# Kernel optimization log

Measured on AMD Instinct MI355X. Metric: run time of the kernel, lower is better.

The kernel has to match this reference:

```python
import jax, jax.numpy as jnp
import numpy as np

V, E, H2 = 32000, 512, 1024  # vocab, embed dim, lstm hidden (hidden_dim*2)
H = 512                      # attention inner dim (hidden_dim)
B, S = 64, 128
L = 2


def _lstm_cell(x, h, c, w_ih, w_hh, b_ih, b_hh):
    # PyTorch gate order: i, f, g, o
    gates = x @ w_ih.T + b_ih + h @ w_hh.T + b_hh
    i, f, g, o = jnp.split(gates, 4, axis=-1)
    i = jax.nn.sigmoid(i); f = jax.nn.sigmoid(f)
    g = jnp.tanh(g); o = jax.nn.sigmoid(o)
    c_new = f * c + i * g
    h_new = o * jnp.tanh(c_new)
    return h_new, c_new


def setup_inputs() -> dict:
    key = jax.random.key(0)
    ks = jax.random.split(key, 20)
    s = 0.05
    inp = {
        'input_token': jax.random.randint(ks[0], (B,), 0, V, dtype=jnp.int32),
        'hidden': jax.random.normal(ks[1], (L, B, H2), jnp.float32),
        'cell': jax.random.normal(ks[2], (L, B, H2), jnp.float32),
        'encoder_outputs': jax.random.normal(ks[3], (B, S, H2), jnp.float32),
        'mask': jax.random.randint(ks[4], (B, S), 0, 2, dtype=jnp.int32),
        'emb_table': jax.random.normal(ks[5], (V, E), jnp.float32) * s,
        'attn_w': jax.random.normal(ks[6], (H, 4 * H), jnp.float32) * s,
        'attn_b': jnp.zeros((H,), jnp.float32),
        'v_w': jax.random.normal(ks[7], (1, H), jnp.float32) * s,
        'w_ih0': jax.random.normal(ks[8], (4 * H2, E + H2), jnp.float32) * s,
        'w_hh0': jax.random.normal(ks[9], (4 * H2, H2), jnp.float32) * s,
        'b_ih0': jnp.zeros((4 * H2,), jnp.float32),
        'b_hh0': jnp.zeros((4 * H2,), jnp.float32),
        'w_ih1': jax.random.normal(ks[10], (4 * H2, H2), jnp.float32) * s,
        'w_hh1': jax.random.normal(ks[11], (4 * H2, H2), jnp.float32) * s,
        'b_ih1': jnp.zeros((4 * H2,), jnp.float32),
        'b_hh1': jnp.zeros((4 * H2,), jnp.float32),
        'fc_w': jax.random.normal(ks[12], (V, 4 * H + E), jnp.float32) * s,
        'fc_b': jnp.zeros((V,), jnp.float32),
    }
    return inp


def reference(input_token, hidden, cell, encoder_outputs, mask,
              emb_table, attn_w, attn_b, v_w,
              w_ih0, w_hh0, b_ih0, b_hh0,
              w_ih1, w_hh1, b_ih1, b_hh1,
              fc_w, fc_b):
    embedded = emb_table[input_token]                       # [B, E]
    h_top = hidden[-1]                                      # [B, 2H]
    # Bahdanau additive attention
    h_rep = jnp.broadcast_to(h_top[:, None, :], (B, S, H2))
    energy = jnp.tanh(jnp.concatenate([h_rep, encoder_outputs], axis=2) @ attn_w.T + attn_b)  # [B,S,H]
    attention = energy @ v_w[0]                             # [B, S]
    attention = jnp.where(mask == 0, jnp.float32(-1e10), attention)
    attn_weights = jax.nn.softmax(attention, axis=1)
    context = jnp.einsum('bs,bsd->bd', attn_weights, encoder_outputs)  # [B, 2H]
    # single-step 2-layer LSTM
    x = jnp.concatenate([embedded, context], axis=1)        # [B, E+2H]
    h0, c0 = _lstm_cell(x, hidden[0], cell[0], w_ih0, w_hh0, b_ih0, b_hh0)
    h1, c1 = _lstm_cell(h0, hidden[1], cell[1], w_ih1, w_hh1, b_ih1, b_hh1)
    new_hidden = jnp.stack([h0, h1])
    new_cell = jnp.stack([c0, c1])
    prediction = jnp.concatenate([h1, context, embedded], axis=1) @ fc_w.T + fc_b  # [B, V]
    return prediction, new_hidden, new_cell, attn_weights
```

## Files before the change

kernel.cpp:

```cpp
#include <hip/hip_runtime.h>


typedef __attribute__((ext_vector_type(8))) short bf16x8;
typedef __attribute__((ext_vector_type(4))) float f32x4;

__device__ __forceinline__ short f2bf(float f){
  __bf16 h = (__bf16)f;
  return __builtin_bit_cast(short, h);
}

__device__ __forceinline__ bf16x8 cvt8(float4 a, float4 b){
  bf16x8 r;
  r[0]=f2bf(a.x); r[1]=f2bf(a.y); r[2]=f2bf(a.z); r[3]=f2bf(a.w);
  r[4]=f2bf(b.x); r[5]=f2bf(b.y); r[6]=f2bf(b.z); r[7]=f2bf(b.w);
  return r;
}

__device__ __forceinline__ bf16x8 ld8_bf(const float* __restrict__ p){
  return cvt8(*(const float4*)p, *(const float4*)(p + 4));
}

__device__ __forceinline__ float fast_tanh(float x){
  x = fminf(fmaxf(x, -15.f), 15.f);
  float t = __expf(2.f * x);
  return (t - 1.f) / (t + 1.f);
}
__device__ __forceinline__ float fast_sig(float x){
  return 1.f / (1.f + __expf(-x));
}

__device__ __forceinline__ void stage16(const void* src, void* dst_lds){
  __builtin_amdgcn_global_load_lds(
      (const __attribute__((address_space(1))) void*)src,
      (__attribute__((address_space(3))) void*)dst_lds, 16, 0, 0);
}

__global__ __launch_bounds__(256) void prep_all(
    const int* __restrict__ tok, const float* __restrict__ emb,
    const float* __restrict__ hidden, const float* __restrict__ enc,
    const float* __restrict__ attn_w,
    short* __restrict__ encbf, short* __restrict__ Wbf,
    short* __restrict__ A0, short* __restrict__ A1, short* __restrict__ Zb,
    float* __restrict__ sco)
{
  const int bid = blockIdx.x, t = threadIdx.x;
  if (bid < 4096){
    long i = ((long)bid*256 + t)*8;
    *(bf16x8*)(encbf + i) = ld8_bf(enc + i);
  } else if (bid < 4352){
    int j = (bid-4096)*256 + t;
    int r = j >> 7, c = (j & 127)*8;
    *(bf16x8*)(Wbf + r*1024 + c) = ld8_bf(attn_w + (long)r*2048 + 1024 + c);
  } else if (bid < 4368){
    int j = (bid-4352)*256 + t;
    int b = j >> 6, e8 = (j & 63)*8;
    bf16x8 v = ld8_bf(emb + (long)tok[b]*512 + e8);
    *(bf16x8*)(A0 + b*2560 + e8) = v;
    *(bf16x8*)(Zb + b*2560 + 2048 + e8) = v;
  } else if (bid < 4400){
    int j = (bid-4368)*256 + t;
    int b = j >> 7, n8 = (j & 127)*8;
    *(bf16x8*)(A0 + b*2560 + 1536 + n8) = ld8_bf(hidden + (long)b*1024 + n8);
    *(bf16x8*)(A1 + b*2048 + 1024 + n8) = ld8_bf(hidden + 65536 + (long)b*1024 + n8);
  } else {
    int j = (bid-4400)*256 + t;
    float4 z = {0.f, 0.f, 0.f, 0.f};
    *(float4*)(sco + j*8) = z;
    *(float4*)(sco + j*8 + 4) = z;
  }
}

#define KSL 256
__global__ __launch_bounds__(256) void gemm_lds(
    const short* __restrict__ A, int lda,
    const float* __restrict__ W1, int sW1, int K1,
    const float* __restrict__ W2, int sW2,
    float* __restrict__ P, int N)
{
  __shared__ short Al[64*256];
  __shared__ float Wl[3][64*64];
  const int wv   = threadIdx.x >> 6;
  const int lane = threadIdx.x & 63;
  const int l15  = lane & 15;
  const int lg   = lane >> 4;
  const int nb   = blockIdx.x * 64;
  const int k0   = blockIdx.y * KSL;

  const float* W; int sW, koff;
  if (k0 < K1){ W = W1; sW = sW1; koff = k0; }
  else        { W = W2; sW = sW2; koff = k0 - K1; }

  {
    const int r2  = lane >> 5;
    const int c16 = (lane & 31) * 16;
    #pragma unroll
    for (int i = 0; i < 8; ++i){
      int rbase = wv*16 + i*2;
      int row   = rbase + r2;
      const char* src = (const char*)A + (long)row*lda*2 + (long)k0*2
                        + (c16 ^ ((row & 7) << 4));
      stage16(src, (void*)(Al + rbase*256));
    }
  }

  auto STAGEW = [&](int bi, int kbase){
    #pragma unroll
    for (int i = 0; i < 4; ++i){
      int row = wv*16 + i*4 + lg;
      const char* src = (const char*)(W + (long)(nb + row)*sW + koff + kbase)
                        + ((l15*16) ^ ((row & 7) << 4));
      stage16(src, (void*)&Wl[bi][(wv*16 + i*4)*64]);
    }
  };

  STAGEW(0, 0);
  STAGEW(1, 64);
  asm volatile("s_waitcnt vmcnt(8)" ::: "memory");
  asm volatile("s_barrier" ::: "memory");

  f32x4 acc[4];
  #pragma unroll
  for (int m = 0; m < 4; ++m) acc[m] = (f32x4){0.f,0.f,0.f,0.f};

  const int  rl = wv*16 + l15;
  const int  sw = (l15 & 7) << 4;
  const char* wbase = (const char*)&Wl[0][0];
  const char* abase = (const char*)Al;

  auto COMPUTE = [&](int bi, int t){
    bf16x8 a[4][2];
    #pragma unroll
    for (int m = 0; m < 4; ++m)
      #pragma unroll
      for (int h = 0; h < 2; ++h){
        int cb = t*128 + h*64 + lg*16;
        a[m][h] = *(const bf16x8*)(abase + (m*16 + l15)*512 + (cb ^ sw));
      }
    const char* rb = wbase + bi*16384 + rl*256;
    float4 w00 = *(const float4*)(rb + ((lg*32      ) ^ sw));
    float4 w01 = *(const float4*)(rb + ((lg*32 + 16 ) ^ sw));
    float4 w10 = *(const float4*)(rb + ((lg*32 + 128) ^ sw));
    float4 w11 = *(const float4*)(rb + ((lg*32 + 144) ^ sw));
    bf16x8 wf0 = cvt8(w00, w01);
    bf16x8 wf1 = cvt8(w10, w11);
    #pragma unroll
    for (int m = 0; m < 4; ++m)
      acc[m] = __builtin_amdgcn_mfma_f32_16x16x32_bf16(a[m][0], wf0, acc[m], 0,0,0);
    #pragma unroll
    for (int m = 0; m < 4; ++m)
      acc[m] = __builtin_amdgcn_mfma_f32_16x16x32_bf16(a[m][1], wf1, acc[m], 0,0,0);
  };

  asm volatile("s_waitcnt vmcnt(4)" ::: "memory");
  COMPUTE(0, 0);
  STAGEW(2, 128);
  asm volatile("s_waitcnt vmcnt(4)" ::: "memory");
  COMPUTE(1, 1);
  STAGEW(0, 192);
  asm volatile("s_waitcnt vmcnt(4)" ::: "memory");
  COMPUTE(2, 2);
  asm volatile("s_waitcnt vmcnt(0)" ::: "memory");
  COMPUTE(0, 3);

  float* p = P + (long)blockIdx.y * 64 * N;
  #pragma unroll
  for (int mt = 0; mt < 4; ++mt)
    #pragma unroll
    for (int r = 0; r < 4; ++r){
      int m = mt*16 + lg*4 + r;
      p[(long)m * N + nb + wv*16 + l15] = acc[mt][r];
    }
}

__global__ __launch_bounds__(256) void gemm_fc2(
    const short* __restrict__ A, int lda,
    const float* __restrict__ W, int sW,
    const float* __restrict__ bias,
    float* __restrict__ C, int N)
{
  __shared__ short Al[2][64*128];
  __shared__ float Wl[3][64*64];
  const int wv   = threadIdx.x >> 6;
  const int lane = threadIdx.x & 63;
  const int l15  = lane & 15;
  const int lg   = lane >> 4;
  const int nb   = blockIdx.x * 64;

  auto STAGEA = [&](int c){
    short* dst = Al[c & 1];
    #pragma unroll
    for (int i = 0; i < 4; ++i){
      int rbase = wv*16 + i*4;
      int row   = rbase + lg;
      const char* src = (const char*)(A + (long)row*lda + c*128)
                        + ((l15*16) ^ ((row & 7) << 4));
      stage16(src, (void*)(dst + rbase*128));
    }
  };
  auto STAGEW = [&](int s){
    float* dst = Wl[s % 3];
    #pragma unroll
    for (int i = 0; i < 4; ++i){
      int row = wv*16 + i*4 + lg;
      const char* src = (const char*)(W + (long)(nb + row)*sW + s*64)
                        + ((l15*16) ^ ((row & 7) << 4));
      stage16(src, (void*)(dst + (wv*16 + i*4)*64));
    }
  };

  f32x4 acc[4];
  #pragma unroll
  for (int m = 0; m < 4; ++m) acc[m] = (f32x4){0.f,0.f,0.f,0.f};

  const int rl = wv*16 + l15;
  const int sw = (l15 & 7) << 4;

  auto COMPUTE = [&](int s){
    const char* abase = (const char*)Al[(s >> 1) & 1];
    const int   kh    = (s & 1) * 128;
    bf16x8 a[4][2];
    #pragma unroll
    for (int m = 0; m < 4; ++m)
      #pragma unroll
      for (int h = 0; h < 2; ++h){
        int cb = kh + h*64 + lg*16;
        a[m][h] = *(const bf16x8*)(abase + (m*16 + l15)*256 + (cb ^ sw));
      }
    const char* rb = (const char*)Wl[s % 3] + rl*256;
    float4 w00 = *(const float4*)(rb + ((lg*32      ) ^ sw));
    float4 w01 = *(const float4*)(rb + ((lg*32 + 16 ) ^ sw));
    float4 w10 = *(const float4*)(rb + ((lg*32 + 128) ^ sw));
    float4 w11 = *(const float4*)(rb + ((lg*32 + 144) ^ sw));
    bf16x8 wf0 = cvt8(w00, w01);
    bf16x8 wf1 = cvt8(w10, w11);
    #pragma unroll
    for (int m = 0; m < 4; ++m)
      acc[m] = __builtin_amdgcn_mfma_f32_16x16x32_bf16(a[m][0], wf0, acc[m], 0,0,0);
    #pragma unroll
    for (int m = 0; m < 4; ++m)
      acc[m] = __builtin_amdgcn_mfma_f32_16x16x32_bf16(a[m][1], wf1, acc[m], 0,0,0);
  };

  STAGEA(0); STAGEW(0); STAGEW(1);
  asm volatile("s_waitcnt vmcnt(4)" ::: "memory");
  __builtin_amdgcn_s_barrier();

  STAGEA(1);
  COMPUTE(0);
  STAGEW(2);
  asm volatile("s_waitcnt vmcnt(4)" ::: "memory");
  COMPUTE(1);
  STAGEW(3);
  __builtin_amdgcn_s_barrier();

  for (int c = 1; c < 19; ++c){
    STAGEA(c+1);
    asm volatile("s_waitcnt vmcnt(8)" ::: "memory");
    COMPUTE(2*c);
    STAGEW(2*c+2);
    asm volatile("s_waitcnt vmcnt(4)" ::: "memory");
    COMPUTE(2*c+1);
    STAGEW(2*c+3);
    __builtin_amdgcn_s_barrier();
  }

  asm volatile("s_waitcnt vmcnt(4)" ::: "memory");
  COMPUTE(38);
  asm volatile("s_waitcnt vmcnt(0)" ::: "memory");
  COMPUTE(39);

  const int col = nb + wv*16 + l15;
  const float bn = bias[col];
  #pragma unroll
  for (int mt = 0; mt < 4; ++mt)
    #pragma unroll
    for (int r = 0; r < 4; ++r){
      int m = mt*16 + lg*4 + r;
      C[(long)m * N + col] = acc[mt][r] + bn;
    }
}

__global__ __launch_bounds__(256) void energy_lds(
    const short* __restrict__ encbf, const short* __restrict__ Wbf,
    const float* __restrict__ Ph, const float* __restrict__ attn_b,
    const float* __restrict__ v_w, float* __restrict__ scores)
{
  __shared__ short Ab[3][64*64];
  __shared__ short Bb[3][64*64];
  const int bx   = blockIdx.x;
  const int m3   = bx & 127, n3 = bx >> 7;
  const int wv   = threadIdx.x >> 6;
  const int lane = threadIdx.x & 63;
  const int l15  = lane & 15;
  const int lg   = lane >> 4;
  const int mb   = m3 * 64;
  const int nbg  = n3 * 64;
  const int nb   = nbg + wv * 16;
  const int b    = mb >> 7;

  const int hi = b*512 + nb + l15;
  const float hp = attn_b[nb + l15] + Ph[hi] + Ph[32768 + hi]
                 + Ph[65536 + hi] + Ph[98304 + hi];
  const float vn = v_w[nb + l15];

  const int srow = lane >> 3;
  const int scb  = (lane & 7) * 16;

  auto STAGE = [&](int c, int kb){
    short* da = Ab[c % 3];
    short* db = Bb[c % 3];
    #pragma unroll
    for (int i = 0; i < 2; ++i){
      int rbase = wv*16 + i*8;
      int row   = rbase + srow;
      int swz   = scb ^ ((row & 7) << 4);
      const char* sa = (const char*)(encbf + (long)(mb + row)*1024 + kb) + swz;
      stage16(sa, (void*)(da + rbase*64));
      const char* sb = (const char*)(Wbf + (long)(nbg + row)*1024 + kb) + swz;
      stage16(sb, (void*)(db + rbase*64));
    }
  };

  f32x4 acc[4] = {};
  const int brow = wv*16 + l15;
  const int bswz = (brow & 7) << 4;
  const int aswz = (l15 & 7) << 4;

  auto COMPUTE = [&](int c){
    const char* ab = (const char*)Ab[c % 3];
    const char* bb = (const char*)Bb[c % 3];
    #pragma unroll
    for (int h = 0; h < 2; ++h){
      const int colb = h*64 + lg*16;
      bf16x8 bf_ = *(const bf16x8*)(bb + brow*128 + (colb ^ bswz));
      #pragma unroll
      for (int m = 0; m < 4; ++m){
        const int arow = m*16 + l15;
        bf16x8 af = *(const bf16x8*)(ab + arow*128 + (colb ^ aswz));
        acc[m] = __builtin_amdgcn_mfma_f32_16x16x32_bf16(af, bf_, acc[m], 0,0,0);
      }
    }
  };

  STAGE(0, 0);
  STAGE(1, 64);
  for (int c = 0; c < 14; ++c){
    asm volatile("s_waitcnt vmcnt(4)" ::: "memory");
    __builtin_amdgcn_s_barrier();
    COMPUTE(c);
    STAGE(c+2, (c+2)*64);
  }
  asm volatile("s_waitcnt vmcnt(4)" ::: "memory");
  __builtin_amdgcn_s_barrier();
  COMPUTE(14);
  asm volatile("s_waitcnt vmcnt(0)" ::: "memory");
  __builtin_amdgcn_s_barrier();
  COMPUTE(15);

  #pragma unroll
  for (int mt = 0; mt < 4; ++mt){
    #pragma unroll
    for (int r = 0; r < 4; ++r){
      int m = mb + mt*16 + lg*4 + r;
      float e = fast_tanh(acc[mt][r] + hp) * vn;
      e += __shfl_xor(e, 1, 16);
      e += __shfl_xor(e, 2, 16);
      e += __shfl_xor(e, 4, 16);
      e += __shfl_xor(e, 8, 16);
      if (l15 == 0) atomicAdd(&scores[m], e);
    }
  }
}

__global__ __launch_bounds__(256) void ctxsm_k(
    const float* __restrict__ sco, const int* __restrict__ mask,
    const short* __restrict__ encbf, float* __restrict__ aw,
    short* __restrict__ A0, short* __restrict__ Zb)
{
  const int bb = blockIdx.x;
  const int t  = threadIdx.x;
  __shared__ float red[128];
  __shared__ float w[128];
  float v = 0.f;
  if (t < 128){
    v = sco[bb*128 + t];
    if (mask[bb*128 + t] == 0) v = -1e10f;
    red[t] = v;
  }
  __syncthreads();
  for (int d = 64; d > 0; d >>= 1){
    if (t < d) red[t] = fmaxf(red[t], red[t + d]);
    __syncthreads();
  }
  const float mx = red[0];
  __syncthreads();
  if (t < 128){
    float e = __expf(v - mx);
    w[t] = e; red[t] = e;
  }
  __syncthreads();
  for (int d = 64; d > 0; d >>= 1){
    if (t < d) red[t] += red[t + d];
    __syncthreads();
  }
  const float inv = 1.f / red[0];
  if (blockIdx.y == 0 && t < 128) aw[bb*128 + t] = w[t] * inv;

  const int dd = blockIdx.y * 256 + t;
  const unsigned short* e = (const unsigned short*)encbf + (long)bb*131072 + dd;
  float s0 = 0.f, s1 = 0.f, s2 = 0.f, s3 = 0.f;
  #pragma unroll 8
  for (int si = 0; si < 128; si += 4){
    s0 += w[si  ] * __builtin_bit_cast(float, (unsigned)e[(si  )*1024] << 16);
    s1 += w[si+1] * __builtin_bit_cast(float, (unsigned)e[(si+1)*1024] << 16);
    s2 += w[si+2] * __builtin_bit_cast(float, (unsigned)e[(si+2)*1024] << 16);
    s3 += w[si+3] * __builtin_bit_cast(float, (unsigned)e[(si+3)*1024] << 16);
  }
  float s = ((s0 + s1) + (s2 + s3)) * inv;
  short vbf = f2bf(s);
  A0[bb*2560 + 512  + dd] = vbf;
  Zb[bb*2560 + 1024 + dd] = vbf;
}

template<int KS>
__global__ __launch_bounds__(256) void lstm_k(
    const float* __restrict__ P,
    const float* __restrict__ bi, const float* __restrict__ bh,
    const float* __restrict__ c_prev,
    float* __restrict__ h_out, float* __restrict__ c_out,
    short* __restrict__ h_bf, int bf_stride)
{
  const int i = blockIdx.x * 256 + threadIdx.x;
  const int b = i >> 10, n = i & 1023;
  float g4[4];
  #pragma unroll
  for (int gi = 0; gi < 4; ++gi){
    int col = gi*1024 + n;
    float s = bi[col] + bh[col];
    const float* p = P + (long)b*4096 + col;
    #pragma unroll
    for (int sl = 0; sl < KS; ++sl) s += p[(long)sl * 262144];
    g4[gi] = s;
  }
  float iv = fast_sig (g4[0]);
  float fv = fast_sig (g4[1]);
  float gv = fast_tanh(g4[2]);
  float ov = fast_sig (g4[3]);
  float c = fv * c_prev[i] + iv * gv;
  float h = ov * fast_tanh(c);
  c_out[i] = c;
  h_out[i] = h;
  h_bf[(long)b * bf_stride + n] = f2bf(h);
}

extern "C" void kernel_launch(void* const* d_in, const int* in_sizes, int n_in,
                              void* d_out, int out_size, void* d_ws, size_t ws_size,
                              hipStream_t stream)
{
  const int*   tok    = (const int*)  d_in[0];
  const float* hidden = (const float*)d_in[1];
  const float* cell   = (const float*)d_in[2];
  const float* enc    = (const float*)d_in[3];
  const int*   mask   = (const int*)  d_in[4];
  const float* emb    = (const float*)d_in[5];
  const float* attn_w = (const float*)d_in[6];
  const float* attn_b = (const float*)d_in[7];
  const float* v_w    = (const float*)d_in[8];
  const float* w_ih0  = (const float*)d_in[9];
  const float* w_hh0  = (const float*)d_in[10];
  const float* b_ih0  = (const float*)d_in[11];
  const float* b_hh0  = (const float*)d_in[12];
  const float* w_ih1  = (const float*)d_in[13];
  const float* w_hh1  = (const float*)d_in[14];
  const float* b_ih1  = (const float*)d_in[15];
  const float* b_hh1  = (const float*)d_in[16];
  const float* fc_w   = (const float*)d_in[17];
  const float* fc_b   = (const float*)d_in[18];

  float* out  = (float*)d_out;
  float* pred = out;
  float* nh   = out + 2048000;
  float* nc   = out + 2179072;
  float* aw   = out + 2310144;

  char*  wsb   = (char*)d_ws;
  short* encbf = (short*)(wsb + 0);
  short* Wbf   = (short*)(wsb + 16777216);
  short* A0    = (short*)(wsb + 17825792);
  short* A1    = (short*)(wsb + 18153472);
  short* Zb    = (short*)(wsb + 18415616);
  float* sco   = (float*)(wsb + 18743296);
  float* Pb    = (float*)(wsb + 18776064);

  prep_all<<<4404, 256, 0, stream>>>(tok, emb, hidden, enc, attn_w,
                                     encbf, Wbf, A0, A1, Zb, sco);

  gemm_lds<<<dim3(8, 4), 256, 0, stream>>>(A1 + 1024, 2048,
                                           attn_w, 2048, 1<<30, nullptr, 0,
                                           Pb, 512);

  energy_lds<<<1024, 256, 0, stream>>>(encbf, Wbf, Pb, attn_b, v_w, sco);

  ctxsm_k<<<dim3(64, 4), 256, 0, stream>>>(sco, mask, encbf, aw, A0, Zb);

  gemm_lds<<<dim3(64, 10), 256, 0, stream>>>(A0, 2560,
                                             w_ih0, 1536, 1536, w_hh0, 1024,
                                             Pb, 4096);
  lstm_k<10><<<256, 256, 0, stream>>>(Pb, b_ih0, b_hh0, cell,
                                      nh, nc, A1, 2048);

  gemm_lds<<<dim3(64, 8), 256, 0, stream>>>(A1, 2048,
                                            w_ih1, 1024, 1024, w_hh1, 1024,
                                            Pb, 4096);
  lstm_k<8><<<256, 256, 0, stream>>>(Pb, b_ih1, b_hh1, cell + 65536,
                                     nh + 65536, nc + 65536, Zb, 2560);

  gemm_fc2<<<500, 256, 0, stream>>>(Zb, 2560, fc_w, 2560, fc_b, pred, 32000);
}
```

Baseline: 147.4 us.

## Split FC GEMM to overlap context/embedding part with layer-0 gates GEMM

```diff
diff --git a/kernel.cpp b/kernel.cpp
--- a/kernel.cpp
+++ b/kernel.cpp
@@ -35,56 +35,18 @@
       (__attribute__((address_space(3))) void*)dst_lds, 16, 0, 0);
 }
 
-__global__ __launch_bounds__(256) void prep_all(
-    const int* __restrict__ tok, const float* __restrict__ emb,
-    const float* __restrict__ hidden, const float* __restrict__ enc,
-    const float* __restrict__ attn_w,
-    short* __restrict__ encbf, short* __restrict__ Wbf,
-    short* __restrict__ A0, short* __restrict__ A1, short* __restrict__ Zb,
-    float* __restrict__ sco)
-{
-  const int bid = blockIdx.x, t = threadIdx.x;
-  if (bid < 4096){
-    long i = ((long)bid*256 + t)*8;
-    *(bf16x8*)(encbf + i) = ld8_bf(enc + i);
-  } else if (bid < 4352){
-    int j = (bid-4096)*256 + t;
-    int r = j >> 7, c = (j & 127)*8;
-    *(bf16x8*)(Wbf + r*1024 + c) = ld8_bf(attn_w + (long)r*2048 + 1024 + c);
-  } else if (bid < 4368){
-    int j = (bid-4352)*256 + t;
-    int b = j >> 6, e8 = (j & 63)*8;
-    bf16x8 v = ld8_bf(emb + (long)tok[b]*512 + e8);
-    *(bf16x8*)(A0 + b*2560 + e8) = v;
-    *(bf16x8*)(Zb + b*2560 + 2048 + e8) = v;
-  } else if (bid < 4400){
-    int j = (bid-4368)*256 + t;
-    int b = j >> 7, n8 = (j & 127)*8;
-    *(bf16x8*)(A0 + b*2560 + 1536 + n8) = ld8_bf(hidden + (long)b*1024 + n8);
-    *(bf16x8*)(A1 + b*2048 + 1024 + n8) = ld8_bf(hidden + 65536 + (long)b*1024 + n8);
-  } else {
-    int j = (bid-4400)*256 + t;
-    float4 z = {0.f, 0.f, 0.f, 0.f};
-    *(float4*)(sco + j*8) = z;
-    *(float4*)(sco + j*8 + 4) = z;
-  }
-}
-
-#define KSL 256
-__global__ __launch_bounds__(256) void gemm_lds(
+__device__ __forceinline__ void gates_body(
     const short* __restrict__ A, int lda,
     const float* __restrict__ W1, int sW1, int K1,
     const float* __restrict__ W2, int sW2,
-    float* __restrict__ P, int N)
-{
-  __shared__ short Al[64*256];
-  __shared__ float Wl[3][64*64];
+    float* __restrict__ Pplane, int N, int nb, int k0, char* smem)
+{
+  short* Al = (short*)smem;
+  float* Wl = (float*)(smem + 32768);
   const int wv   = threadIdx.x >> 6;
   const int lane = threadIdx.x & 63;
   const int l15  = lane & 15;
   const int lg   = lane >> 4;
-  const int nb   = blockIdx.x * 64;
-  const int k0   = blockIdx.y * KSL;
 
   const float* W; int sW, koff;
   if (k0 < K1){ W = W1; sW = sW1; koff = k0; }
@@ -109,7 +71,7 @@
       int row = wv*16 + i*4 + lg;
       const char* src = (const char*)(W + (long)(nb + row)*sW + koff + kbase)
                         + ((l15*16) ^ ((row & 7) << 4));
-      stage16(src, (void*)&Wl[bi][(wv*16 + i*4)*64]);
+      stage16(src, (void*)(Wl + bi*4096 + (wv*16 + i*4)*64));
     }
   };
 
@@ -124,7 +86,7 @@
 
   const int  rl = wv*16 + l15;
   const int  sw = (l15 & 7) << 4;
-  const char* wbase = (const char*)&Wl[0][0];
+  const char* wbase = (const char*)Wl;
   const char* abase = (const char*)Al;
 
   auto COMPUTE = [&](int bi, int t){
@@ -162,32 +124,30 @@
   asm volatile("s_waitcnt vmcnt(0)" ::: "memory");
   COMPUTE(0, 3);
 
-  float* p = P + (long)blockIdx.y * 64 * N;
   #pragma unroll
   for (int mt = 0; mt < 4; ++mt)
     #pragma unroll
     for (int r = 0; r < 4; ++r){
       int m = mt*16 + lg*4 + r;
-      p[(long)m * N + nb + wv*16 + l15] = acc[mt][r];
-    }
-}
-
-__global__ __launch_bounds__(256) void gemm_fc2(
+      Pplane[(long)m * N + nb + wv*16 + l15] = acc[mt][r];
+    }
+}
+
+__device__ __forceinline__ void fc_body(
     const short* __restrict__ A, int lda,
-    const float* __restrict__ W, int sW,
-    const float* __restrict__ bias,
-    float* __restrict__ C, int N)
-{
-  __shared__ short Al[2][64*128];
-  __shared__ float Wl[3][64*64];
+    const float* __restrict__ W, int sW, int NC,
+    const float* __restrict__ addsrc, const float* __restrict__ bias,
+    float* __restrict__ C, int N, int nb, char* smem)
+{
+  short* Al = (short*)smem;
+  float* Wl = (float*)(smem + 32768);
   const int wv   = threadIdx.x >> 6;
   const int lane = threadIdx.x & 63;
   const int l15  = lane & 15;
   const int lg   = lane >> 4;
-  const int nb   = blockIdx.x * 64;
 
   auto STAGEA = [&](int c){
-    short* dst = Al[c & 1];
+    short* dst = Al + (c & 1) * 8192;
     #pragma unroll
     for (int i = 0; i < 4; ++i){
       int rbase = wv*16 + i*4;
@@ -198,7 +158,7 @@
     }
   };
   auto STAGEW = [&](int s){
-    float* dst = Wl[s % 3];
+    float* dst = Wl + (s % 3) * 4096;
     #pragma unroll
     for (int i = 0; i < 4; ++i){
       int row = wv*16 + i*4 + lg;
@@ -216,7 +176,7 @@
   const int sw = (l15 & 7) << 4;
 
   auto COMPUTE = [&](int s){
-    const char* abase = (const char*)Al[(s >> 1) & 1];
+    const char* abase = (const char*)(Al + ((s >> 1) & 1) * 8192);
     const int   kh    = (s & 1) * 128;
     bf16x8 a[4][2];
     #pragma unroll
@@ -226,7 +186,7 @@
         int cb = kh + h*64 + lg*16;
         a[m][h] = *(const bf16x8*)(abase + (m*16 + l15)*256 + (cb ^ sw));
       }
-    const char* rb = (const char*)Wl[s % 3] + rl*256;
+    const char* rb = (const char*)(Wl + (s % 3)*4096) + rl*256;
     float4 w00 = *(const float4*)(rb + ((lg*32      ) ^ sw));
     float4 w01 = *(const float4*)(rb + ((lg*32 + 16 ) ^ sw));
     float4 w10 = *(const float4*)(rb + ((lg*32 + 128) ^ sw));
@@ -253,7 +213,7 @@
   STAGEW(3);
   __builtin_amdgcn_s_barrier();
 
-  for (int c = 1; c < 19; ++c){
+  for (int c = 1; c < NC-1; ++c){
     STAGEA(c+1);
     asm volatile("s_waitcnt vmcnt(8)" ::: "memory");
     COMPUTE(2*c);
@@ -265,25 +225,96 @@
   }
 
   asm volatile("s_waitcnt vmcnt(4)" ::: "memory");
-  COMPUTE(38);
+  COMPUTE(2*NC-2);
   asm volatile("s_waitcnt vmcnt(0)" ::: "memory");
-  COMPUTE(39);
+  COMPUTE(2*NC-1);
 
   const int col = nb + wv*16 + l15;
-  const float bn = bias[col];
+  const float bn = bias ? bias[col] : 0.f;
   #pragma unroll
   for (int mt = 0; mt < 4; ++mt)
     #pragma unroll
     for (int r = 0; r < 4; ++r){
       int m = mt*16 + lg*4 + r;
-      C[(long)m * N + col] = acc[mt][r] + bn;
-    }
+      long idx = (long)m * N + col;
+      float v = acc[mt][r] + bn;
+      if (addsrc) v += addsrc[idx];
+      C[idx] = v;
+    }
+}
+
+__global__ __launch_bounds__(256) void prep_all(
+    const int* __restrict__ tok, const float* __restrict__ emb,
+    const float* __restrict__ hidden, const float* __restrict__ enc,
+    const float* __restrict__ attn_w, const float* __restrict__ attn_b,
+    short* __restrict__ encbf, short* __restrict__ Wbf,
+    short* __restrict__ A0, short* __restrict__ A1, short* __restrict__ Zb,
+    float* __restrict__ sco, float* __restrict__ hpr)
+{
+  const int bid = blockIdx.x, t = threadIdx.x;
+  if (bid < 8){
+    const int wv = t >> 6, lane = t & 63, l15 = lane & 15, lg = lane >> 4;
+    const int nb = bid*64 + wv*16;
+    const float* hrow = hidden + 65536;
+    const float* wrow = attn_w + (long)(nb + l15)*2048 + lg*8;
+    f32x4 acc[4] = {};
+    bf16x8 wn  = ld8_bf(wrow);
+    bf16x8 an0 = ld8_bf(hrow + l15*1024 + lg*8);
+    bf16x8 an1 = ld8_bf(hrow + (16+l15)*1024 + lg*8);
+    bf16x8 an2 = ld8_bf(hrow + (32+l15)*1024 + lg*8);
+    bf16x8 an3 = ld8_bf(hrow + (48+l15)*1024 + lg*8);
+    for (int kb = 32; kb < 1024; kb += 32){
+      bf16x8 wc = wn, c0 = an0, c1 = an1, c2 = an2, c3 = an3;
+      wn  = ld8_bf(wrow + kb);
+      an0 = ld8_bf(hrow + l15*1024 + lg*8 + kb);
+      an1 = ld8_bf(hrow + (16+l15)*1024 + lg*8 + kb);
+      an2 = ld8_bf(hrow + (32+l15)*1024 + lg*8 + kb);
+      an3 = ld8_bf(hrow + (48+l15)*1024 + lg*8 + kb);
+      acc[0] = __builtin_amdgcn_mfma_f32_16x16x32_bf16(c0, wc, acc[0], 0,0,0);
+      acc[1] = __builtin_amdgcn_mfma_f32_16x16x32_bf16(c1, wc, acc[1], 0,0,0);
+      acc[2] = __builtin_amdgcn_mfma_f32_16x16x32_bf16(c2, wc, acc[2], 0,0,0);
+      acc[3] = __builtin_amdgcn_mfma_f32_16x16x32_bf16(c3, wc, acc[3], 0,0,0);
+    }
+    acc[0] = __builtin_amdgcn_mfma_f32_16x16x32_bf16(an0, wn, acc[0], 0,0,0);
+    acc[1] = __builtin_amdgcn_mfma_f32_16x16x32_bf16(an1, wn, acc[1], 0,0,0);
+    acc[2] = __builtin_amdgcn_mfma_f32_16x16x32_bf16(an2, wn, acc[2], 0,0,0);
+    acc[3] = __builtin_amdgcn_mfma_f32_16x16x32_bf16(an3, wn, acc[3], 0,0,0);
+    const float bn = attn_b[nb + l15];
+    #pragma unroll
+    for (int mt = 0; mt < 4; ++mt)
+      #pragma unroll
+      for (int r = 0; r < 4; ++r)
+        hpr[(mt*16 + lg*4 + r)*512 + nb + l15] = acc[mt][r] + bn;
+  } else if (bid < 4104){
+    long i = ((long)(bid-8)*256 + t)*8;
+    *(bf16x8*)(encbf + i) = ld8_bf(enc + i);
+  } else if (bid < 4360){
+    int j = (bid-4104)*256 + t;
+    int r = j >> 7, c = (j & 127)*8;
+    *(bf16x8*)(Wbf + r*1024 + c) = ld8_bf(attn_w + (long)r*2048 + 1024 + c);
+  } else if (bid < 4376){
+    int j = (bid-4360)*256 + t;
+    int b = j >> 6, e8 = (j & 63)*8;
+    bf16x8 v = ld8_bf(emb + (long)tok[b]*512 + e8);
+    *(bf16x8*)(A0 + b*2560 + e8) = v;
+    *(bf16x8*)(Zb + b*2560 + 2048 + e8) = v;
+  } else if (bid < 4408){
+    int j = (bid-4376)*256 + t;
+    int b = j >> 7, n8 = (j & 127)*8;
+    *(bf16x8*)(A0 + b*2560 + 1536 + n8) = ld8_bf(hidden + (long)b*1024 + n8);
+    *(bf16x8*)(A1 + b*2048 + 1024 + n8) = ld8_bf(hidden + 65536 + (long)b*1024 + n8);
+  } else {
+    int j = (bid-4408)*256 + t;
+    float4 z = {0.f, 0.f, 0.f, 0.f};
+    *(float4*)(sco + j*8) = z;
+    *(float4*)(sco + j*8 + 4) = z;
+  }
 }
 
 __global__ __launch_bounds__(256) void energy_lds(
     const short* __restrict__ encbf, const short* __restrict__ Wbf,
-    const float* __restrict__ Ph, const float* __restrict__ attn_b,
-    const float* __restrict__ v_w, float* __restrict__ scores)
+    const float* __restrict__ hpr, const float* __restrict__ v_w,
+    float* __restrict__ scores)
 {
   __shared__ short Ab[3][64*64];
   __shared__ short Bb[3][64*64];
@@ -298,9 +329,7 @@
   const int nb   = nbg + wv * 16;
   const int b    = mb >> 7;
 
-  const int hi = b*512 + nb + l15;
-  const float hp = attn_b[nb + l15] + Ph[hi] + Ph[32768 + hi]
-                 + Ph[65536 + hi] + Ph[98304 + hi];
+  const float hp = hpr[(long)b*512 + nb + l15];
   const float vn = v_w[nb + l15];
 
   const int srow = lane >> 3;
@@ -420,6 +449,46 @@
   short vbf = f2bf(s);
   A0[bb*2560 + 512  + dd] = vbf;
   Zb[bb*2560 + 1024 + dd] = vbf;
+}
+
+__global__ __launch_bounds__(256) void gemm_lds(
+    const short* __restrict__ A, int lda,
+    const float* __restrict__ W1, int sW1, int K1,
+    const float* __restrict__ W2, int sW2,
+    float* __restrict__ P, int N)
+{
+  __shared__ char smem[81920];
+  gates_body(A, lda, W1, sW1, K1, W2, sW2,
+             P + (long)blockIdx.y * 64 * N, N,
+             blockIdx.x * 64, blockIdx.y * 256, smem);
+}
+
+__global__ __launch_bounds__(256) void combo_k(
+    const short* __restrict__ A0, const float* __restrict__ w_ih0,
+    const float* __restrict__ w_hh0, float* __restrict__ Pb,
+    const short* __restrict__ Zb, const float* __restrict__ fc_w,
+    float* __restrict__ predP)
+{
+  __shared__ char smem[81920];
+  if (blockIdx.x < 500){
+    fc_body(Zb + 1024, 2560, fc_w + 1024, 2560, 12, nullptr, nullptr,
+            predP, 32000, blockIdx.x * 64, smem);
+  } else {
+    int b2 = blockIdx.x - 500;
+    gates_body(A0, 2560, w_ih0, 1536, 1536, w_hh0, 1024,
+               Pb + (long)(b2 >> 6) * 262144, 4096,
+               (b2 & 63) * 64, (b2 >> 6) * 256, smem);
+  }
+}
+
+__global__ __launch_bounds__(256) void fc_final(
+    const short* __restrict__ Zb, const float* __restrict__ fc_w,
+    const float* __restrict__ predP, const float* __restrict__ fc_b,
+    float* __restrict__ pred)
+{
+  __shared__ char smem[81920];
+  fc_body(Zb, 2560, fc_w, 2560, 8, predP, fc_b, pred, 32000,
+          blockIdx.x * 64, smem);
 }
 
 template<int KS>
@@ -490,22 +559,19 @@
   short* A1    = (short*)(wsb + 18153472);
   short* Zb    = (short*)(wsb + 18415616);
   float* sco   = (float*)(wsb + 18743296);
-  float* Pb    = (float*)(wsb + 18776064);
-
-  prep_all<<<4404, 256, 0, stream>>>(tok, emb, hidden, enc, attn_w,
-                                     encbf, Wbf, A0, A1, Zb, sco);
-
-  gemm_lds<<<dim3(8, 4), 256, 0, stream>>>(A1 + 1024, 2048,
-                                           attn_w, 2048, 1<<30, nullptr, 0,
-                                           Pb, 512);
-
-  energy_lds<<<1024, 256, 0, stream>>>(encbf, Wbf, Pb, attn_b, v_w, sco);
+  float* hpr   = (float*)(wsb + 18776064);
+  float* Pb    = (float*)(wsb + 18907136);
+  float* predP = (float*)(wsb + 29392896);
+
+  prep_all<<<4412, 256, 0, stream>>>(tok, emb, hidden, enc, attn_w, attn_b,
+                                     encbf, Wbf, A0, A1, Zb, sco, hpr);
+
+  energy_lds<<<1024, 256, 0, stream>>>(encbf, Wbf, hpr, v_w, sco);
 
   ctxsm_k<<<dim3(64, 4), 256, 0, stream>>>(sco, mask, encbf, aw, A0, Zb);
 
-  gemm_lds<<<dim3(64, 10), 256, 0, stream>>>(A0, 2560,
-                                             w_ih0, 1536, 1536, w_hh0, 1024,
-                                             Pb, 4096);
+  combo_k<<<1140, 256, 0, stream>>>(A0, w_ih0, w_hh0, Pb, Zb, fc_w, predP);
+
   lstm_k<10><<<256, 256, 0, stream>>>(Pb, b_ih0, b_hh0, cell,
                                       nh, nc, A1, 2048);
 
@@ -515,5 +581,5 @@
   lstm_k<8><<<256, 256, 0, stream>>>(Pb, b_ih1, b_hh1, cell + 65536,
                                      nh + 65536, nc + 65536, Zb, 2560);
 
-  gemm_fc2<<<500, 256, 0, stream>>>(Zb, 2560, fc_w, 2560, fc_b, pred, 32000);
-}
+  fc_final<<<500, 256, 0, stream>>>(Zb, fc_w, predP, fc_b, pred);
+}
```

New measurement: 175.3 us. 1.19x slower.
